# Kernel optimization log

Measured on AMD Instinct MI355X. Metric: run time of the kernel, lower is better.

Reference implementation:

```python
import jax, jax.numpy as jnp
import numpy as np

B, L, H, M, E, NH, R = 4, 512, 1024, 128, 64, 16, 1024   # docs, seq, hidden, mentions, entities, heads, pairs
D, BLK, C = 768, 64, 97                                   # embed_size, block_size, num_class


def setup_inputs() -> dict:
    key = jax.random.key(0)
    ks = jax.random.split(key, 9)
    seq_lhs = jax.random.normal(ks[0], (B, L, H), jnp.float32)
    ent_lhs = jax.random.normal(ks[1], (B, M, H), jnp.float32)
    ent_to_seq_attn = jax.random.uniform(ks[2], (B, NH, M, L), jnp.float32)
    entity_id_labels = jax.random.randint(ks[3], (B, M), 0, E, jnp.int32)
    hts = jax.random.randint(ks[4], (B, R, 2), 0, E, jnp.int32)
    Wh = jax.random.normal(ks[5], (2 * H, D), jnp.float32) * 0.02
    Wt = jax.random.normal(ks[6], (2 * H, D), jnp.float32) * 0.02
    Wb = jax.random.normal(ks[7], (D * BLK, C), jnp.float32) * 0.02
    return dict(seq_lhs=seq_lhs, ent_lhs=ent_lhs, ent_to_seq_attn=ent_to_seq_attn,
                entity_id_labels=entity_id_labels, hts=hts,
                Wh=Wh, bh=jnp.zeros((D,), jnp.float32),
                Wt=Wt, bt=jnp.zeros((D,), jnp.float32),
                Wb=Wb, bb=jnp.zeros((C,), jnp.float32))


def reference(seq_lhs, ent_lhs, ent_to_seq_attn, entity_id_labels, hts, Wh, bh, Wt, bt, Wb, bb):
    # --- hrt_pool: segment logsumexp / mean over mentions per entity ---
    mask = entity_id_labels[:, None, :] == jnp.arange(E, dtype=entity_id_labels.dtype)[None, :, None]  # [B,E,M]
    cnt = mask.sum(-1)  # [B,E]
    neg = jnp.asarray(-1e30, ent_lhs.dtype)
    masked = jnp.where(mask[..., None], ent_lhs[:, None, :, :], neg)          # [B,E,M,H]
    lse = jax.nn.logsumexp(masked, axis=2)                                    # [B,E,H]
    ent_emb = jnp.where((cnt > 0)[..., None], lse, 0.0)
    mf = mask.astype(ent_to_seq_attn.dtype)
    attn_sum = jnp.einsum('bem,bhml->behl', mf, ent_to_seq_attn)              # [B,E,NH,L]
    denom = jnp.maximum(cnt, 1).astype(attn_sum.dtype)[..., None, None]
    ent_attn = jnp.where((cnt > 0)[..., None, None], attn_sum / denom, 0.0)
    # --- gather head/tail entities per pair ---
    h_idx, t_idx = hts[..., 0], hts[..., 1]                                   # [B,R]
    hs = jnp.take_along_axis(ent_emb, h_idx[..., None], axis=1)               # [B,R,H]
    ts = jnp.take_along_axis(ent_emb, t_idx[..., None], axis=1)
    h_attn = jnp.take_along_axis(ent_attn, h_idx[..., None, None], axis=1)    # [B,R,NH,L]
    t_attn = jnp.take_along_axis(ent_attn, t_idx[..., None, None], axis=1)
    ht_attn = (h_attn * t_attn).mean(axis=2)                                  # [B,R,L]
    ht_attn = ht_attn / (ht_attn.sum(-1, keepdims=True) + 1e-5)
    rel = jnp.einsum('brl,bld->brd', ht_attn, seq_lhs)                        # [B,R,H]
    # --- extractors + block bilinear ---
    hcat = jnp.concatenate([hs, rel], -1).reshape(B * R, 2 * H)
    tcat = jnp.concatenate([ts, rel], -1).reshape(B * R, 2 * H)
    hv = jnp.tanh(hcat @ Wh + bh)
    tv = jnp.tanh(tcat @ Wt + bt)
    b1 = hv.reshape(-1, D // BLK, BLK)
    b2 = tv.reshape(-1, D // BLK, BLK)
    bl = (b1[:, :, :, None] * b2[:, :, None, :]).reshape(-1, D * BLK)
    return bl @ Wb + bb                                                       # [B*R, C]
```

## Files before the change

### kernel.cpp

```cpp
#include <hip/hip_runtime.h>
#include <hip/hip_bf16.h>
#include <math.h>

#define B_  4
#define L_  512
#define H_  1024
#define M_  128
#define E_  64
#define NH_ 16
#define R_  1024
#define D_  768
#define BLK_ 64
#define C_  97
#define NROW (B_*R_)
#define KB_  (D_/BLK_)

typedef __attribute__((ext_vector_type(8))) unsigned short ushort8;
typedef __attribute__((ext_vector_type(4))) unsigned short ushort4v;
typedef __attribute__((ext_vector_type(8))) short s8;
typedef __attribute__((ext_vector_type(4))) float f4;

__device__ __forceinline__ unsigned short f2bf(float x) {
    unsigned u = __builtin_bit_cast(unsigned, x);
    unsigned r = (u + 0x7fffu + ((u >> 16) & 1u)) >> 16;
    return (unsigned short)r;
}
__device__ __forceinline__ float bf2f(unsigned short h) {
    unsigned u = ((unsigned)h) << 16;
    return __builtin_bit_cast(float, u);
}
__device__ __forceinline__ float lo16f(unsigned u) { return __builtin_bit_cast(float, u << 16); }
__device__ __forceinline__ float hi16f(unsigned u) { return __builtin_bit_cast(float, u & 0xffff0000u); }

__device__ __forceinline__ void gload_lds16(const unsigned short* g, unsigned short* l)
{
    __builtin_amdgcn_global_load_lds(
        (const __attribute__((address_space(1))) unsigned int*)g,
        (__attribute__((address_space(3))) unsigned int*)l, 16, 0, 0);
}

__global__ __launch_bounds__(256) void pool_lse(
    const float* __restrict__ ent_lhs, const int* __restrict__ labels,
    unsigned short* __restrict__ ent_embB)
{
    int be = blockIdx.x, b = be >> 6, e = be & 63;
    __shared__ int midx[M_];
    __shared__ int scnt;
    if (threadIdx.x == 0) scnt = 0;
    __syncthreads();
    if (threadIdx.x < M_) {
        if (labels[b*M_ + threadIdx.x] == e) {
            int p = atomicAdd(&scnt, 1);
            midx[p] = threadIdx.x;
        }
    }
    __syncthreads();
    int cnt = scnt;
    for (int h = threadIdx.x; h < H_; h += blockDim.x) {
        float r = 0.f;
        if (cnt > 0) {
            const float* base = ent_lhs + (size_t)b*M_*H_ + h;
            float mx = -INFINITY;
            for (int k = 0; k < cnt; ++k) mx = fmaxf(mx, base[(size_t)midx[k]*H_]);
            float s = 0.f;
            for (int k = 0; k < cnt; ++k) s += expf(base[(size_t)midx[k]*H_] - mx);
            r = mx + logf(s);
        }
        ent_embB[(size_t)be*H_ + h] = f2bf(r);
    }
}

__global__ __launch_bounds__(256) void pool_attn(
    const float* __restrict__ attn, const int* __restrict__ labels,
    unsigned short* __restrict__ ent_attnB)
{
    int e  = blockIdx.x;
    int y  = blockIdx.y;
    int b  = y >> 4, nh = y & 15;
    __shared__ int midx[M_];
    __shared__ int scnt;
    if (threadIdx.x == 0) scnt = 0;
    __syncthreads();
    if (threadIdx.x < M_) {
        if (labels[b*M_ + threadIdx.x] == e) {
            int p = atomicAdd(&scnt, 1);
            midx[p] = threadIdx.x;
        }
    }
    __syncthreads();
    int cnt = scnt;
    float inv = (cnt > 0) ? 1.f/(float)cnt : 0.f;
    const float* base = attn + ((size_t)(b*NH_ + nh)*M_)*L_;
    #pragma unroll
    for (int q = 0; q < 2; ++q) {
        int l = threadIdx.x + q*256;
        float s = 0.f;
        for (int k = 0; k < cnt; ++k) s += base[(size_t)midx[k]*L_ + l];
        ent_attnB[((size_t)(b*E_ + e)*NH_ + nh)*L_ + l] = f2bf(s * inv);
    }
}

__global__ __launch_bounds__(256) void pair_attn_kernel(
    const unsigned short* __restrict__ entA, const int* __restrict__ hts,
    unsigned short* __restrict__ htA)
{
    int w  = threadIdx.x >> 6, ln = threadIdx.x & 63;
    int br = blockIdx.x*4 + w, b = br >> 10;
    int hi = hts[br*2 + 0], ti = hts[br*2 + 1];
    const unsigned* ph = (const unsigned*)(entA + ((size_t)(b*E_ + hi)*NH_)*L_);
    const unsigned* pt = (const unsigned*)(entA + ((size_t)(b*E_ + ti)*NH_)*L_);
    float v0[4] = {0.f, 0.f, 0.f, 0.f};
    float v1[4] = {0.f, 0.f, 0.f, 0.f};
    #pragma unroll
    for (int nh = 0; nh < NH_; ++nh) {
        #pragma unroll
        for (int c = 0; c < 4; ++c) {
            int l2 = ln + c*64;
            unsigned a = ph[nh*(L_/2) + l2], d = pt[nh*(L_/2) + l2];
            v0[c] += lo16f(a)*lo16f(d);
            v1[c] += hi16f(a)*hi16f(d);
        }
    }
    float part = 0.f;
    #pragma unroll
    for (int c = 0; c < 4; ++c) part += v0[c] + v1[c];
    #pragma unroll
    for (int off = 32; off > 0; off >>= 1) part += __shfl_xor(part, off, 64);
    float norm = 1.f / (part*(1.f/16.f) + 1e-5f);
    #pragma unroll
    for (int c = 0; c < 4; ++c) {
        unsigned short o0 = f2bf(v0[c]*(1.f/16.f)*norm);
        unsigned short o1 = f2bf(v1[c]*(1.f/16.f)*norm);
        *(unsigned*)(htA + (size_t)br*L_ + (size_t)(ln + c*64)*2) = ((unsigned)o1 << 16) | o0;
    }
}

__global__ __launch_bounds__(256) void cvt_seq(const float* __restrict__ in,
                                               unsigned short* __restrict__ outp)
{
    size_t i = ((size_t)blockIdx.x*256 + threadIdx.x) * 8;
    float4 a = *(const float4*)(in + i);
    float4 b = *(const float4*)(in + i + 4);
    ushort8 o = { f2bf(a.x), f2bf(a.y), f2bf(a.z), f2bf(a.w),
                  f2bf(b.x), f2bf(b.y), f2bf(b.z), f2bf(b.w) };
    *(ushort8*)(outp + i) = o;
}

__global__ __launch_bounds__(256) void transpose_cvt_W(const float* __restrict__ Wh,
                                                       const float* __restrict__ Wt,
                                                       unsigned short* __restrict__ WhT,
                                                       unsigned short* __restrict__ WtT)
{
    const float* in = blockIdx.z ? Wt : Wh;
    unsigned short* outp = blockIdx.z ? WtT : WhT;
    int n0 = blockIdx.x*32, k0 = blockIdx.y*32;
    __shared__ float tile[32][33];
    int tx = threadIdx.x & 31, ty = threadIdx.x >> 5;
    #pragma unroll
    for (int p = 0; p < 4; ++p)
        tile[ty + p*8][tx] = in[((size_t)(k0 + ty + p*8))*D_ + n0 + tx];
    __syncthreads();
    #pragma unroll
    for (int p = 0; p < 4; ++p) {
        int n = n0 + ty + p*8;
        outp[(size_t)n*2048 + k0 + tx] = f2bf(tile[tx][ty + p*8]);
    }
}

__global__ __launch_bounds__(256) void prep_WbT(const float* __restrict__ Wb,
                                                unsigned short* __restrict__ outp)
{
    int blk = blockIdx.x;
    __shared__ float sW[64*97];
    const float* src = Wb + (size_t)blk*64*97;
    for (int e = threadIdx.x; e < 64*97; e += 256) sW[e] = src[e];
    __syncthreads();
    unsigned short* dst = outp + (size_t)blk*128*64;
    for (int e = threadIdx.x; e < 128*64; e += 256) {
        int wcq = e >> 12;
        int ct  = (e >> 10) & 3;
        int j2  = (e >> 9) & 1;
        int qd  = (e >> 7) & 3;
        int lm  = (e >> 3) & 15;
        int t   = e & 7;
        int c   = wcq*64 + ct*16 + lm;
        int j   = j2*32 + qd*8 + t;
        dst[e] = (c < C_) ? f2bf(sW[j*97 + c]) : (unsigned short)0;
    }
}

__device__ __forceinline__ void gemm128_core(const unsigned short* __restrict__ A, int lda,
                                             const unsigned short* __restrict__ Bt, int ldb,
                                             int K, int row0, int col0,
                                             f4 (&acc)[4][4])
{
    __shared__ __attribute__((aligned(16))) unsigned short As[128][32];
    __shared__ __attribute__((aligned(16))) unsigned short Bs[128][32];
    int tid = threadIdx.x;
    int wave = tid >> 6, lane = tid & 63;
    int wr = wave & 1, wc = wave >> 1;
    int lm = lane & 15, quad = lane >> 4;

    for (int k0 = 0; k0 < K; k0 += 32) {
        #pragma unroll
        for (int s = 0; s < 2; ++s) {
            int ch = tid + s*256;
            int row = ch >> 2, part = ch & 3;
            gload_lds16(A  + (size_t)(row0 + row)*lda + k0 + part*8, &As[0][0] + ch*8);
            gload_lds16(Bt + (size_t)(col0 + row)*ldb + k0 + part*8, &Bs[0][0] + ch*8);
        }
        __syncthreads();
        s8 a[4], b[4];
        #pragma unroll
        for (int ti = 0; ti < 4; ++ti) a[ti] = *(const s8*)&As[wr*64 + ti*16 + lm][quad*8];
        #pragma unroll
        for (int tj = 0; tj < 4; ++tj) b[tj] = *(const s8*)&Bs[wc*64 + tj*16 + lm][quad*8];
        #pragma unroll
        for (int ti = 0; ti < 4; ++ti)
            #pragma unroll
            for (int tj = 0; tj < 4; ++tj)
                acc[ti][tj] = __builtin_amdgcn_mfma_f32_16x16x32_bf16(a[ti], b[tj], acc[ti][tj], 0, 0, 0);
        __syncthreads();
    }
}

__global__ __launch_bounds__(256) void gemm_swt_mfma(
    const unsigned short* __restrict__ seqB,
    const unsigned short* __restrict__ WhT, const unsigned short* __restrict__ WtT,
    unsigned short* __restrict__ SWT)
{
    int bz = blockIdx.z, z = bz >> 2, b = bz & 3;
    const unsigned short* A  = (z ? WtT : WhT) + 1024;
    const unsigned short* Bt = seqB + (size_t)b*L_*H_;
    int row0 = blockIdx.y*128, col0 = blockIdx.x*128;
    f4 acc[4][4] = {};
    gemm128_core(A, 2048, Bt, H_, H_, row0, col0, acc);
    unsigned short* Cb = SWT + ((size_t)(z*B_ + b)*D_)*L_;
    int lane = threadIdx.x & 63, wave = threadIdx.x >> 6;
    int wr = wave & 1, wc = wave >> 1, lm = lane & 15, quad = lane >> 4;
    #pragma unroll
    for (int ti = 0; ti < 4; ++ti)
        #pragma unroll
        for (int tj = 0; tj < 4; ++tj)
            #pragma unroll
            for (int r = 0; r < 4; ++r) {
                int d = row0 + wr*64 + ti*16 + quad*4 + r;
                int l = col0 + wc*64 + tj*16 + lm;
                Cb[(size_t)d*L_ + l] = f2bf(acc[ti][tj][r]);
            }
}

__global__ __launch_bounds__(256) void gemm_p_mfma(
    const unsigned short* __restrict__ ent_embB,
    const unsigned short* __restrict__ WhT, const unsigned short* __restrict__ WtT,
    float* __restrict__ Ph, float* __restrict__ Pt)
{
    int z = blockIdx.z;
    const unsigned short* Bt = z ? WtT : WhT;
    float* P = z ? Pt : Ph;
    int mt = blockIdx.y & 1, ks = blockIdx.y >> 1;
    int row0 = mt*128, col0 = blockIdx.x*128;
    f4 acc[4][4] = {};
    gemm128_core(ent_embB + ks*256, H_, Bt + ks*256, 2048, 256, row0, col0, acc);
    int lane = threadIdx.x & 63, wave = threadIdx.x >> 6;
    int wr = wave & 1, wc = wave >> 1, lm = lane & 15, quad = lane >> 4;
    #pragma unroll
    for (int ti = 0; ti < 4; ++ti)
        #pragma unroll
        for (int tj = 0; tj < 4; ++tj)
            #pragma unroll
            for (int r = 0; r < 4; ++r) {
                int row = row0 + wr*64 + ti*16 + quad*4 + r;
                int col = col0 + wc*64 + tj*16 + lm;
                atomicAdd(P + (size_t)row*D_ + col, acc[ti][tj][r]);
            }
}

__global__ __launch_bounds__(256) void gemm_ext_mfma(
    const unsigned short* __restrict__ htA,
    const unsigned short* __restrict__ SWT,
    const float* __restrict__ Ph, const float* __restrict__ Pt,
    const int* __restrict__ hts,
    unsigned short* __restrict__ hvB, unsigned short* __restrict__ tvB)
{
    int z = blockIdx.z;
    const float* P = z ? Pt : Ph;
    unsigned short* Cv = z ? tvB : hvB;
    int row0 = blockIdx.y*128, col0 = blockIdx.x*128;
    int b = row0 >> 10;
    const unsigned short* Bt = SWT + ((size_t)(z*B_ + b)*D_)*L_;
    f4 acc[4][4] = {};
    gemm128_core(htA, L_, Bt, L_, L_, row0, col0, acc);
    int lane = threadIdx.x & 63, wave = threadIdx.x >> 6;
    int wr = wave & 1, wc = wave >> 1, lm = lane & 15, quad = lane >> 4;
    #pragma unroll
    for (int ti = 0; ti < 4; ++ti)
        #pragma unroll
        for (int r = 0; r < 4; ++r) {
            int row = row0 + wr*64 + ti*16 + quad*4 + r;
            int idx = hts[row*2 + z];
            const float* prow = P + ((size_t)(b*E_ + idx))*D_;
            #pragma unroll
            for (int tj = 0; tj < 4; ++tj) {
                int col = col0 + wc*64 + tj*16 + lm;
                float x = acc[ti][tj][r] + prow[col];
                float e = __expf(2.f*x);
                Cv[(size_t)row*D_ + col] = f2bf(1.f - 2.f/(e + 1.f));
            }
        }
}

__global__ void out_init(const float* __restrict__ bb,
                         const float* __restrict__ bh, const float* __restrict__ bt,
                         float* __restrict__ out,
                         float* __restrict__ Ph, float* __restrict__ Pt)
{
    int i = blockIdx.x*256 + threadIdx.x;
    if (i < NROW*C_) out[i] = bb[i % C_];
    if (i < 256*D_) {
        Ph[i] = bh[i % D_];
        Pt[i] = bt[i % D_];
    }
}

__device__ __forceinline__ void loadB_frag(const unsigned short* __restrict__ bbase,
                                           int i, s8 (&dst)[4][2])
{
    #pragma unroll
    for (int ct = 0; ct < 4; ++ct) {
        dst[ct][0] = *(const s8*)(bbase + (size_t)i*8192 + ct*1024);
        dst[ct][1] = *(const s8*)(bbase + (size_t)i*8192 + ct*1024 + 512);
    }
}

__device__ __forceinline__ void compute_i4(const s8 (&bfr)[4][2],
                                           const float (&sh)[4],
                                           const float (&tvv)[4][2][8],
                                           f4 (&acc)[4][4])
{
    s8 afr[4][2];
    #pragma unroll
    for (int rt = 0; rt < 4; ++rt)
        #pragma unroll
        for (int j2 = 0; j2 < 2; ++j2) {
            union { unsigned u[4]; s8 v; } cv;
            #pragma unroll
            for (int t2 = 0; t2 < 4; ++t2) {
                float pe = sh[rt] * tvv[rt][j2][t2*2];
                float po = sh[rt] * tvv[rt][j2][t2*2 + 1];
                cv.u[t2] = __builtin_amdgcn_perm(__builtin_bit_cast(unsigned, po),
                                                 __builtin_bit_cast(unsigned, pe),
                                                 0x07060302u);
            }
            afr[rt][j2] = cv.v;
        }
    #pragma unroll
    for (int ct = 0; ct < 4; ++ct)
        #pragma unroll
        for (int rt = 0; rt < 4; ++rt) {
            acc[rt][ct] = __builtin_amdgcn_mfma_f32_16x16x32_bf16(afr[rt][0], bfr[ct][0], acc[rt][ct], 0, 0, 0);
            acc[rt][ct] = __builtin_amdgcn_mfma_f32_16x16x32_bf16(afr[rt][1], bfr[ct][1], acc[rt][ct], 0, 0, 0);
        }
}

__global__ __launch_bounds__(256) void final_mfma(
    const unsigned short* __restrict__ hvB,
    const unsigned short* __restrict__ tvB,
    const unsigned short* __restrict__ WbT,
    float* __restrict__ out)
{
    int kb   = blockIdx.x;
    int row0 = blockIdx.y * 128;
    __shared__ __attribute__((aligned(16))) unsigned short hS[128][72];
    __shared__ __attribute__((aligned(16))) unsigned short tS[128][72];

    int tid = threadIdx.x;
    for (int e = tid; e < 1024; e += 256) {
        int r = e >> 3, part = e & 7;
        *(ushort8*)&hS[r][part*8] = *(const ushort8*)(hvB + (size_t)(row0 + r)*D_ + kb*BLK_ + part*8);
        *(ushort8*)&tS[r][part*8] = *(const ushort8*)(tvB + (size_t)(row0 + r)*D_ + kb*BLK_ + part*8);
    }
    int wave = tid >> 6, lane = tid & 63;
    int wr = wave & 1, wc = wave >> 1;
    int lm = lane & 15, quad = lane >> 4;
    __syncthreads();

    float tvv[4][2][8];
    #pragma unroll
    for (int rt = 0; rt < 4; ++rt)
        #pragma unroll
        for (int j2 = 0; j2 < 2; ++j2) {
            int r = wr*64 + rt*16 + lm;
            ushort8 w = *(const ushort8*)&tS[r][j2*32 + quad*8];
            #pragma unroll
            for (int t = 0; t < 8; ++t) tvv[rt][j2][t] = bf2f(w[t]);
        }

    f4 acc[4][4] = {};
    const unsigned short* bbase = WbT + (size_t)kb*(64*128*64)
                                + (size_t)wc*4096 + ((size_t)quad*16 + lm)*8;

    s8 bufA[4][2], bufB[4][2];
    loadB_frag(bbase, 0, bufA);
    for (int i0 = 0; i0 < 64; i0 += 2) {
        loadB_frag(bbase, i0 + 1, bufB);
        {
            float sh[4];
            #pragma unroll
            for (int rt = 0; rt < 4; ++rt) sh[rt] = bf2f(hS[wr*64 + rt*16 + lm][i0]);
            compute_i4(bufA, sh, tvv, acc);
        }
        if (i0 < 62) loadB_frag(bbase, i0 + 2, bufA);
        {
            float sh[4];
            #pragma unroll
            for (int rt = 0; rt < 4; ++rt) sh[rt] = bf2f(hS[wr*64 + rt*16 + lm][i0 + 1]);
            compute_i4(bufB, sh, tvv, acc);
        }
    }

    #pragma unroll
    for (int rt = 0; rt < 4; ++rt)
        #pragma unroll
        for (int ct = 0; ct < 4; ++ct)
            #pragma unroll
            for (int r = 0; r < 4; ++r) {
                int row = row0 + wr*64 + rt*16 + quad*4 + r;
                int col = wc*64 + ct*16 + lm;
                if (col < C_) atomicAdd(out + (size_t)row*C_ + col, acc[rt][ct][r]);
            }
}

extern "C" void kernel_launch(void* const* d_in, const int* in_sizes, int n_in,
                              void* d_out, int out_size, void* d_ws, size_t ws_size,
                              hipStream_t stream)
{
    const float* seq_lhs = (const float*)d_in[0];
    const float* ent_lhs = (const float*)d_in[1];
    const float* attn    = (const float*)d_in[2];
    const int*   labels  = (const int*)d_in[3];
    const int*   hts     = (const int*)d_in[4];
    const float* Wh      = (const float*)d_in[5];
    const float* bh      = (const float*)d_in[6];
    const float* Wt      = (const float*)d_in[7];
    const float* bt      = (const float*)d_in[8];
    const float* Wb      = (const float*)d_in[9];
    const float* bb      = (const float*)d_in[10];
    float* out = (float*)d_out;

    float* wsf      = (float*)d_ws;
    float* Ph       = wsf;
    float* Pt       = Ph + 196608;
    unsigned short* hvB       = (unsigned short*)(Pt + 196608);
    unsigned short* tvB       = hvB       + 3145728;
    unsigned short* ent_embB  = tvB       + 3145728;
    unsigned short* ent_attnB = ent_embB  + 262144;
    unsigned short* htA       = ent_attnB + 2097152;
    unsigned short* seqB      = htA       + 2097152;
    unsigned short* WhT       = seqB      + 2097152;
    unsigned short* WtT       = WhT       + 1572864;
    unsigned short* SWT       = WtT       + 1572864;
    unsigned short* WbT       = SWT       + 3145728;

    transpose_cvt_W<<<dim3(24, 64, 2), 256, 0, stream>>>(Wh, Wt, WhT, WtT);
    prep_WbT<<<KB_*64, 256, 0, stream>>>(Wb, WbT);
    cvt_seq<<<1024, 256, 0, stream>>>(seq_lhs, seqB);

    pool_lse<<<B_*E_, 256, 0, stream>>>(ent_lhs, labels, ent_embB);
    out_init<<<(NROW*C_ + 255)/256, 256, 0, stream>>>(bb, bh, bt, out, Ph, Pt);
    gemm_p_mfma<<<dim3(6, 8, 2), 256, 0, stream>>>(ent_embB, WhT, WtT, Ph, Pt);
    gemm_swt_mfma<<<dim3(4, 6, 8), 256, 0, stream>>>(seqB, WhT, WtT, SWT);
    pool_attn<<<dim3(E_, B_*NH_), 256, 0, stream>>>(attn, labels, ent_attnB);
    pair_attn_kernel<<<B_*R_/4, 256, 0, stream>>>(ent_attnB, hts, htA);
    gemm_ext_mfma<<<dim3(6, 32, 2), 256, 0, stream>>>(htA, SWT, Ph, Pt, hts, hvB, tvB);
    final_mfma<<<dim3(KB_, NROW/128), 256, 0, stream>>>(hvB, tvB, WbT, out);
}
```

Baseline: 280.3 us.

## Merge independent prep and mid-stage kernels into two block-dispatched launches

```diff
diff --git a/kernel.cpp b/kernel.cpp
--- a/kernel.cpp
+++ b/kernel.cpp
@@ -39,153 +39,122 @@
         (__attribute__((address_space(3))) unsigned int*)l, 16, 0, 0);
 }
 
-__global__ __launch_bounds__(256) void pool_lse(
+
+__global__ __launch_bounds__(256) void fused_prep(
+    const float* __restrict__ Wh, const float* __restrict__ Wt,
+    unsigned short* __restrict__ WhT, unsigned short* __restrict__ WtT,
+    const float* __restrict__ Wb, unsigned short* __restrict__ WbT,
+    const float* __restrict__ seq_lhs, unsigned short* __restrict__ seqB,
     const float* __restrict__ ent_lhs, const int* __restrict__ labels,
-    unsigned short* __restrict__ ent_embB)
-{
-    int be = blockIdx.x, b = be >> 6, e = be & 63;
-    __shared__ int midx[M_];
-    __shared__ int scnt;
-    if (threadIdx.x == 0) scnt = 0;
-    __syncthreads();
-    if (threadIdx.x < M_) {
-        if (labels[b*M_ + threadIdx.x] == e) {
-            int p = atomicAdd(&scnt, 1);
-            midx[p] = threadIdx.x;
-        }
-    }
-    __syncthreads();
-    int cnt = scnt;
-    for (int h = threadIdx.x; h < H_; h += blockDim.x) {
-        float r = 0.f;
-        if (cnt > 0) {
-            const float* base = ent_lhs + (size_t)b*M_*H_ + h;
-            float mx = -INFINITY;
-            for (int k = 0; k < cnt; ++k) mx = fmaxf(mx, base[(size_t)midx[k]*H_]);
+    unsigned short* __restrict__ ent_embB,
+    const float* __restrict__ attn, unsigned short* __restrict__ ent_attnB,
+    const float* __restrict__ bb, const float* __restrict__ bh,
+    const float* __restrict__ bt,
+    float* __restrict__ out, float* __restrict__ Ph, float* __restrict__ Pt)
+{
+    __shared__ __attribute__((aligned(16))) float smem[6208];
+    int bx = blockIdx.x, tid = threadIdx.x;
+
+    if (bx < 3072) {
+        int z = bx / 1536, rem = bx % 1536;
+        int ky = rem / 24, kx = rem % 24;
+        const float* in = z ? Wt : Wh;
+        unsigned short* outp = z ? WtT : WhT;
+        int n0 = kx*32, k0 = ky*32;
+        float (*tile)[33] = (float(*)[33])smem;
+        int tx = tid & 31, ty = tid >> 5;
+        #pragma unroll
+        for (int p = 0; p < 4; ++p)
+            tile[ty + p*8][tx] = in[((size_t)(k0 + ty + p*8))*D_ + n0 + tx];
+        __syncthreads();
+        #pragma unroll
+        for (int p = 0; p < 4; ++p) {
+            int n = n0 + ty + p*8;
+            outp[(size_t)n*2048 + k0 + tx] = f2bf(tile[tx][ty + p*8]);
+        }
+    } else if (bx < 3840) {
+        int blk = bx - 3072;
+        float* sW = smem;
+        const float* src = Wb + (size_t)blk*64*97;
+        for (int e = tid; e < 64*97; e += 256) sW[e] = src[e];
+        __syncthreads();
+        unsigned short* dst = WbT + (size_t)blk*128*64;
+        for (int e = tid; e < 128*64; e += 256) {
+            int wcq = e >> 12;
+            int ct  = (e >> 10) & 3;
+            int j2  = (e >> 9) & 1;
+            int qd  = (e >> 7) & 3;
+            int lm  = (e >> 3) & 15;
+            int t   = e & 7;
+            int c   = wcq*64 + ct*16 + lm;
+            int j   = j2*32 + qd*8 + t;
+            dst[e] = (c < C_) ? f2bf(sW[j*97 + c]) : (unsigned short)0;
+        }
+    } else if (bx < 4864) {
+        size_t i = ((size_t)(bx - 3840)*256 + tid) * 8;
+        float4 a = *(const float4*)(seq_lhs + i);
+        float4 b = *(const float4*)(seq_lhs + i + 4);
+        ushort8 o = { f2bf(a.x), f2bf(a.y), f2bf(a.z), f2bf(a.w),
+                      f2bf(b.x), f2bf(b.y), f2bf(b.z), f2bf(b.w) };
+        *(ushort8*)(seqB + i) = o;
+    } else if (bx < 5120) {
+        int be = bx - 4864, b = be >> 6, e = be & 63;
+        int* midx = (int*)smem;
+        int* scnt = (int*)smem + M_;
+        if (tid == 0) *scnt = 0;
+        __syncthreads();
+        if (tid < M_) {
+            if (labels[b*M_ + tid] == e) {
+                int p = atomicAdd(scnt, 1);
+                midx[p] = tid;
+            }
+        }
+        __syncthreads();
+        int cnt = *scnt;
+        for (int h = tid; h < H_; h += 256) {
+            float r = 0.f;
+            if (cnt > 0) {
+                const float* base = ent_lhs + (size_t)b*M_*H_ + h;
+                float mx = -INFINITY;
+                for (int k = 0; k < cnt; ++k) mx = fmaxf(mx, base[(size_t)midx[k]*H_]);
+                float s = 0.f;
+                for (int k = 0; k < cnt; ++k) s += expf(base[(size_t)midx[k]*H_] - mx);
+                r = mx + logf(s);
+            }
+            ent_embB[(size_t)be*H_ + h] = f2bf(r);
+        }
+    } else if (bx < 9216) {
+        int id = bx - 5120;
+        int e = id & 63, y = id >> 6;
+        int b = y >> 4, nh = y & 15;
+        int* midx = (int*)smem;
+        int* scnt = (int*)smem + M_;
+        if (tid == 0) *scnt = 0;
+        __syncthreads();
+        if (tid < M_) {
+            if (labels[b*M_ + tid] == e) {
+                int p = atomicAdd(scnt, 1);
+                midx[p] = tid;
+            }
+        }
+        __syncthreads();
+        int cnt = *scnt;
+        float inv = (cnt > 0) ? 1.f/(float)cnt : 0.f;
+        const float* base = attn + ((size_t)(b*NH_ + nh)*M_)*L_;
+        #pragma unroll
+        for (int q = 0; q < 2; ++q) {
+            int l = tid + q*256;
             float s = 0.f;
-            for (int k = 0; k < cnt; ++k) s += expf(base[(size_t)midx[k]*H_] - mx);
-            r = mx + logf(s);
-        }
-        ent_embB[(size_t)be*H_ + h] = f2bf(r);
-    }
-}
-
-__global__ __launch_bounds__(256) void pool_attn(
-    const float* __restrict__ attn, const int* __restrict__ labels,
-    unsigned short* __restrict__ ent_attnB)
-{
-    int e  = blockIdx.x;
-    int y  = blockIdx.y;
-    int b  = y >> 4, nh = y & 15;
-    __shared__ int midx[M_];
-    __shared__ int scnt;
-    if (threadIdx.x == 0) scnt = 0;
-    __syncthreads();
-    if (threadIdx.x < M_) {
-        if (labels[b*M_ + threadIdx.x] == e) {
-            int p = atomicAdd(&scnt, 1);
-            midx[p] = threadIdx.x;
-        }
-    }
-    __syncthreads();
-    int cnt = scnt;
-    float inv = (cnt > 0) ? 1.f/(float)cnt : 0.f;
-    const float* base = attn + ((size_t)(b*NH_ + nh)*M_)*L_;
-    #pragma unroll
-    for (int q = 0; q < 2; ++q) {
-        int l = threadIdx.x + q*256;
-        float s = 0.f;
-        for (int k = 0; k < cnt; ++k) s += base[(size_t)midx[k]*L_ + l];
-        ent_attnB[((size_t)(b*E_ + e)*NH_ + nh)*L_ + l] = f2bf(s * inv);
-    }
-}
-
-__global__ __launch_bounds__(256) void pair_attn_kernel(
-    const unsigned short* __restrict__ entA, const int* __restrict__ hts,
-    unsigned short* __restrict__ htA)
-{
-    int w  = threadIdx.x >> 6, ln = threadIdx.x & 63;
-    int br = blockIdx.x*4 + w, b = br >> 10;
-    int hi = hts[br*2 + 0], ti = hts[br*2 + 1];
-    const unsigned* ph = (const unsigned*)(entA + ((size_t)(b*E_ + hi)*NH_)*L_);
-    const unsigned* pt = (const unsigned*)(entA + ((size_t)(b*E_ + ti)*NH_)*L_);
-    float v0[4] = {0.f, 0.f, 0.f, 0.f};
-    float v1[4] = {0.f, 0.f, 0.f, 0.f};
-    #pragma unroll
-    for (int nh = 0; nh < NH_; ++nh) {
-        #pragma unroll
-        for (int c = 0; c < 4; ++c) {
-            int l2 = ln + c*64;
-            unsigned a = ph[nh*(L_/2) + l2], d = pt[nh*(L_/2) + l2];
-            v0[c] += lo16f(a)*lo16f(d);
-            v1[c] += hi16f(a)*hi16f(d);
-        }
-    }
-    float part = 0.f;
-    #pragma unroll
-    for (int c = 0; c < 4; ++c) part += v0[c] + v1[c];
-    #pragma unroll
-    for (int off = 32; off > 0; off >>= 1) part += __shfl_xor(part, off, 64);
-    float norm = 1.f / (part*(1.f/16.f) + 1e-5f);
-    #pragma unroll
-    for (int c = 0; c < 4; ++c) {
-        unsigned short o0 = f2bf(v0[c]*(1.f/16.f)*norm);
-        unsigned short o1 = f2bf(v1[c]*(1.f/16.f)*norm);
-        *(unsigned*)(htA + (size_t)br*L_ + (size_t)(ln + c*64)*2) = ((unsigned)o1 << 16) | o0;
-    }
-}
-
-__global__ __launch_bounds__(256) void cvt_seq(const float* __restrict__ in,
-                                               unsigned short* __restrict__ outp)
-{
-    size_t i = ((size_t)blockIdx.x*256 + threadIdx.x) * 8;
-    float4 a = *(const float4*)(in + i);
-    float4 b = *(const float4*)(in + i + 4);
-    ushort8 o = { f2bf(a.x), f2bf(a.y), f2bf(a.z), f2bf(a.w),
-                  f2bf(b.x), f2bf(b.y), f2bf(b.z), f2bf(b.w) };
-    *(ushort8*)(outp + i) = o;
-}
-
-__global__ __launch_bounds__(256) void transpose_cvt_W(const float* __restrict__ Wh,
-                                                       const float* __restrict__ Wt,
-                                                       unsigned short* __restrict__ WhT,
-                                                       unsigned short* __restrict__ WtT)
-{
-    const float* in = blockIdx.z ? Wt : Wh;
-    unsigned short* outp = blockIdx.z ? WtT : WhT;
-    int n0 = blockIdx.x*32, k0 = blockIdx.y*32;
-    __shared__ float tile[32][33];
-    int tx = threadIdx.x & 31, ty = threadIdx.x >> 5;
-    #pragma unroll
-    for (int p = 0; p < 4; ++p)
-        tile[ty + p*8][tx] = in[((size_t)(k0 + ty + p*8))*D_ + n0 + tx];
-    __syncthreads();
-    #pragma unroll
-    for (int p = 0; p < 4; ++p) {
-        int n = n0 + ty + p*8;
-        outp[(size_t)n*2048 + k0 + tx] = f2bf(tile[tx][ty + p*8]);
-    }
-}
-
-__global__ __launch_bounds__(256) void prep_WbT(const float* __restrict__ Wb,
-                                                unsigned short* __restrict__ outp)
-{
-    int blk = blockIdx.x;
-    __shared__ float sW[64*97];
-    const float* src = Wb + (size_t)blk*64*97;
-    for (int e = threadIdx.x; e < 64*97; e += 256) sW[e] = src[e];
-    __syncthreads();
-    unsigned short* dst = outp + (size_t)blk*128*64;
-    for (int e = threadIdx.x; e < 128*64; e += 256) {
-        int wcq = e >> 12;
-        int ct  = (e >> 10) & 3;
-        int j2  = (e >> 9) & 1;
-        int qd  = (e >> 7) & 3;
-        int lm  = (e >> 3) & 15;
-        int t   = e & 7;
-        int c   = wcq*64 + ct*16 + lm;
-        int j   = j2*32 + qd*8 + t;
-        dst[e] = (c < C_) ? f2bf(sW[j*97 + c]) : (unsigned short)0;
+            for (int k = 0; k < cnt; ++k) s += base[(size_t)midx[k]*L_ + l];
+            ent_attnB[((size_t)(b*E_ + e)*NH_ + nh)*L_ + l] = f2bf(s * inv);
+        }
+    } else {
+        int i = (bx - 9216)*256 + tid;
+        if (i < NROW*C_) out[i] = bb[i % C_];
+        if (i < 256*D_) {
+            Ph[i] = bh[i % D_];
+            Pt[i] = bt[i % D_];
+        }
     }
 }
 
@@ -224,56 +193,89 @@
     }
 }
 
-__global__ __launch_bounds__(256) void gemm_swt_mfma(
-    const unsigned short* __restrict__ seqB,
-    const unsigned short* __restrict__ WhT, const unsigned short* __restrict__ WtT,
-    unsigned short* __restrict__ SWT)
-{
-    int bz = blockIdx.z, z = bz >> 2, b = bz & 3;
-    const unsigned short* A  = (z ? WtT : WhT) + 1024;
-    const unsigned short* Bt = seqB + (size_t)b*L_*H_;
-    int row0 = blockIdx.y*128, col0 = blockIdx.x*128;
-    f4 acc[4][4] = {};
-    gemm128_core(A, 2048, Bt, H_, H_, row0, col0, acc);
-    unsigned short* Cb = SWT + ((size_t)(z*B_ + b)*D_)*L_;
-    int lane = threadIdx.x & 63, wave = threadIdx.x >> 6;
-    int wr = wave & 1, wc = wave >> 1, lm = lane & 15, quad = lane >> 4;
-    #pragma unroll
-    for (int ti = 0; ti < 4; ++ti)
-        #pragma unroll
-        for (int tj = 0; tj < 4; ++tj)
-            #pragma unroll
-            for (int r = 0; r < 4; ++r) {
-                int d = row0 + wr*64 + ti*16 + quad*4 + r;
-                int l = col0 + wc*64 + tj*16 + lm;
-                Cb[(size_t)d*L_ + l] = f2bf(acc[ti][tj][r]);
-            }
-}
-
-__global__ __launch_bounds__(256) void gemm_p_mfma(
+__global__ __launch_bounds__(256) void fused_mid(
     const unsigned short* __restrict__ ent_embB,
     const unsigned short* __restrict__ WhT, const unsigned short* __restrict__ WtT,
-    float* __restrict__ Ph, float* __restrict__ Pt)
-{
-    int z = blockIdx.z;
-    const unsigned short* Bt = z ? WtT : WhT;
-    float* P = z ? Pt : Ph;
-    int mt = blockIdx.y & 1, ks = blockIdx.y >> 1;
-    int row0 = mt*128, col0 = blockIdx.x*128;
-    f4 acc[4][4] = {};
-    gemm128_core(ent_embB + ks*256, H_, Bt + ks*256, 2048, 256, row0, col0, acc);
-    int lane = threadIdx.x & 63, wave = threadIdx.x >> 6;
-    int wr = wave & 1, wc = wave >> 1, lm = lane & 15, quad = lane >> 4;
-    #pragma unroll
-    for (int ti = 0; ti < 4; ++ti)
-        #pragma unroll
-        for (int tj = 0; tj < 4; ++tj)
-            #pragma unroll
-            for (int r = 0; r < 4; ++r) {
-                int row = row0 + wr*64 + ti*16 + quad*4 + r;
-                int col = col0 + wc*64 + tj*16 + lm;
-                atomicAdd(P + (size_t)row*D_ + col, acc[ti][tj][r]);
-            }
+    float* __restrict__ Ph, float* __restrict__ Pt,
+    const unsigned short* __restrict__ seqB, unsigned short* __restrict__ SWT,
+    const unsigned short* __restrict__ entA, const int* __restrict__ hts,
+    unsigned short* __restrict__ htA)
+{
+    int bx = blockIdx.x;
+    if (bx < 96) {
+        int x = bx % 6, y = (bx / 6) % 8, z = bx / 48;
+        const unsigned short* Bt = z ? WtT : WhT;
+        float* P = z ? Pt : Ph;
+        int mt = y & 1, ks = y >> 1;
+        int row0 = mt*128, col0 = x*128;
+        f4 acc[4][4] = {};
+        gemm128_core(ent_embB + ks*256, H_, Bt + ks*256, 2048, 256, row0, col0, acc);
+        int lane = threadIdx.x & 63, wave = threadIdx.x >> 6;
+        int wr = wave & 1, wc = wave >> 1, lm = lane & 15, quad = lane >> 4;
+        #pragma unroll
+        for (int ti = 0; ti < 4; ++ti)
+            #pragma unroll
+            for (int tj = 0; tj < 4; ++tj)
+                #pragma unroll
+                for (int r = 0; r < 4; ++r) {
+                    int row = row0 + wr*64 + ti*16 + quad*4 + r;
+                    int col = col0 + wc*64 + tj*16 + lm;
+                    atomicAdd(P + (size_t)row*D_ + col, acc[ti][tj][r]);
+                }
+    } else if (bx < 288) {
+        int id = bx - 96;
+        int x = id % 4, y = (id / 4) % 6, bz = id / 24;
+        int z = bz >> 2, b = bz & 3;
+        const unsigned short* A  = (z ? WtT : WhT) + 1024;
+        const unsigned short* Bt = seqB + (size_t)b*L_*H_;
+        int row0 = y*128, col0 = x*128;
+        f4 acc[4][4] = {};
+        gemm128_core(A, 2048, Bt, H_, H_, row0, col0, acc);
+        unsigned short* Cb = SWT + ((size_t)(z*B_ + b)*D_)*L_;
+        int lane = threadIdx.x & 63, wave = threadIdx.x >> 6;
+        int wr = wave & 1, wc = wave >> 1, lm = lane & 15, quad = lane >> 4;
+        #pragma unroll
+        for (int ti = 0; ti < 4; ++ti)
+            #pragma unroll
+            for (int tj = 0; tj < 4; ++tj)
+                #pragma unroll
+                for (int r = 0; r < 4; ++r) {
+                    int d = row0 + wr*64 + ti*16 + quad*4 + r;
+                    int l = col0 + wc*64 + tj*16 + lm;
+                    Cb[(size_t)d*L_ + l] = f2bf(acc[ti][tj][r]);
+                }
+    } else {
+        int id = bx - 288;
+        int w  = threadIdx.x >> 6, ln = threadIdx.x & 63;
+        int br = id*4 + w, b = br >> 10;
+        int hi = hts[br*2 + 0], ti = hts[br*2 + 1];
+        const unsigned* ph = (const unsigned*)(entA + ((size_t)(b*E_ + hi)*NH_)*L_);
+        const unsigned* pt = (const unsigned*)(entA + ((size_t)(b*E_ + ti)*NH_)*L_);
+        float v0[4] = {0.f, 0.f, 0.f, 0.f};
+        float v1[4] = {0.f, 0.f, 0.f, 0.f};
+        #pragma unroll
+        for (int nh = 0; nh < NH_; ++nh) {
+            #pragma unroll
+            for (int c = 0; c < 4; ++c) {
+                int l2 = ln + c*64;
+                unsigned a = ph[nh*(L_/2) + l2], d = pt[nh*(L_/2) + l2];
+                v0[c] += lo16f(a)*lo16f(d);
+                v1[c] += hi16f(a)*hi16f(d);
+            }
+        }
+        float part = 0.f;
+        #pragma unroll
+        for (int c = 0; c < 4; ++c) part += v0[c] + v1[c];
+        #pragma unroll
+        for (int off = 32; off > 0; off >>= 1) part += __shfl_xor(part, off, 64);
+        float norm = 1.f / (part*(1.f/16.f) + 1e-5f);
+        #pragma unroll
+        for (int c = 0; c < 4; ++c) {
+            unsigned short o0 = f2bf(v0[c]*(1.f/16.f)*norm);
+            unsigned short o1 = f2bf(v1[c]*(1.f/16.f)*norm);
+            *(unsigned*)(htA + (size_t)br*L_ + (size_t)(ln + c*64)*2) = ((unsigned)o1 << 16) | o0;
+        }
+    }
 }
 
 __global__ __launch_bounds__(256) void gemm_ext_mfma(
@@ -308,19 +310,6 @@
                 Cv[(size_t)row*D_ + col] = f2bf(1.f - 2.f/(e + 1.f));
             }
         }
-}
-
-__global__ void out_init(const float* __restrict__ bb,
-                         const float* __restrict__ bh, const float* __restrict__ bt,
-                         float* __restrict__ out,
-                         float* __restrict__ Ph, float* __restrict__ Pt)
-{
-    int i = blockIdx.x*256 + threadIdx.x;
-    if (i < NROW*C_) out[i] = bb[i % C_];
-    if (i < 256*D_) {
-        Ph[i] = bh[i % D_];
-        Pt[i] = bt[i % D_];
-    }
 }
 
 __device__ __forceinline__ void loadB_frag(const unsigned short* __restrict__ bbase,
@@ -462,16 +451,11 @@
     unsigned short* SWT       = WtT       + 1572864;
     unsigned short* WbT       = SWT       + 3145728;
 
-    transpose_cvt_W<<<dim3(24, 64, 2), 256, 0, stream>>>(Wh, Wt, WhT, WtT);
-    prep_WbT<<<KB_*64, 256, 0, stream>>>(Wb, WbT);
-    cvt_seq<<<1024, 256, 0, stream>>>(seq_lhs, seqB);
-
-    pool_lse<<<B_*E_, 256, 0, stream>>>(ent_lhs, labels, ent_embB);
-    out_init<<<(NROW*C_ + 255)/256, 256, 0, stream>>>(bb, bh, bt, out, Ph, Pt);
-    gemm_p_mfma<<<dim3(6, 8, 2), 256, 0, stream>>>(ent_embB, WhT, WtT, Ph, Pt);
-    gemm_swt_mfma<<<dim3(4, 6, 8), 256, 0, stream>>>(seqB, WhT, WtT, SWT);
-    pool_attn<<<dim3(E_, B_*NH_), 256, 0, stream>>>(attn, labels, ent_attnB);
-    pair_attn_kernel<<<B_*R_/4, 256, 0, stream>>>(ent_attnB, hts, htA);
+    fused_prep<<<10768, 256, 0, stream>>>(Wh, Wt, WhT, WtT, Wb, WbT,
+                                          seq_lhs, seqB, ent_lhs, labels, ent_embB,
+                                          attn, ent_attnB, bb, bh, bt, out, Ph, Pt);
+    fused_mid<<<1312, 256, 0, stream>>>(ent_embB, WhT, WtT, Ph, Pt,
+                                        seqB, SWT, ent_attnB, hts, htA);
     gemm_ext_mfma<<<dim3(6, 32, 2), 256, 0, stream>>>(htA, SWT, Ph, Pt, hts, hvB, tvB);
     final_mfma<<<dim3(KB_, NROW/128), 256, 0, stream>>>(hvB, tvB, WbT, out);
 }
```

Result: faster. 244.5 us, median of 2 (-12.8%).
